# Performance work log

Measured on AMD Instinct MI355X. Metric: run time of the kernel, lower is better.

The kernel has to match this reference:

```python
import jax, jax.numpy as jnp
import numpy as np

EPS = 1e-8  # torch.nn.CosineSimilarity eps


def setup_inputs() -> dict:
    key = jax.random.key(0)
    k1, k2, k3 = jax.random.split(key, 3)
    C, S, D = 1024, 16, 512
    x = jax.random.normal(k1, (C, S, D), dtype=jnp.float32)
    w = jax.random.normal(k2, (1,), dtype=jnp.float32)
    b = jax.random.normal(k3, (1,), dtype=jnp.float32)
    return {"x": x, "w": w, "b": b}


def reference(x, w, b):
    # stable_ge2e: leave-one-out positive centroids, full negative centroids.
    C, S, D = x.shape
    wp = jax.nn.softplus(w)  # (1,)

    sum_c = x.sum(axis=1)                      # (C, D)
    mean_c = sum_c / S                         # negative centroids (C, D)
    loo = (sum_c[:, None, :] - x) / (S - 1.0)  # leave-one-out centroids (C, S, D)

    nx = jnp.linalg.norm(x, axis=-1)           # (C, S)
    nmean = jnp.linalg.norm(mean_c, axis=-1)   # (C,)
    nloo = jnp.linalg.norm(loo, axis=-1)       # (C, S)

    # cosine similarities (clamped denominator, as in torch CosineSimilarity)
    sim_neg = jnp.einsum('jid,kd->jik', x, mean_c) / jnp.maximum(
        nx[:, :, None] * nmean[None, None, :], EPS)          # (C, S, C)
    sim_pos = jnp.einsum('jid,jid->ji', x, loo) / jnp.maximum(nx * nloo, EPS)  # (C, S)

    # on the diagonal k == j use the leave-one-out positive centroid
    eye = jnp.eye(C, dtype=bool)
    sim = jnp.where(eye[:, None, :], sim_pos[:, :, None], sim_neg)  # (C, S, C)

    logits = wp * sim + b
    logS = jax.nn.log_softmax(logits, axis=-1)
    Sji_j = jnp.einsum('jij->ji', logS)                        # (C, S) diagonal
    Sji_k = jax.scipy.special.logsumexp(logS, axis=-1)         # (C, S) (== 0 post-softmax)
    loss = -(Sji_j - Sji_k).reshape(-1)
    return loss.mean()
```

## Files before the change

kernel.cpp:

```cpp
#include <hip/hip_runtime.h>
#include <math.h>

#define CC 1024
#define SS 16
#define DD 512
#define RR (CC*SS)
#define EPSV 1e-8f
#define LDB 520
#define LDX 516
#define CHUNK 32
#define NCHUNK 16

typedef __attribute__((ext_vector_type(8))) short short8;
typedef __attribute__((ext_vector_type(4))) float f32x4;
typedef unsigned short ushort_t;

__device__ __forceinline__ unsigned short f2bf(float f) {
  unsigned u = __float_as_uint(f);
  u += 0x7fffu + ((u >> 16) & 1u);
  return (unsigned short)(u >> 16);
}

__device__ __forceinline__ void async16(void* l, const void* g) {
  __builtin_amdgcn_global_load_lds(
      (const __attribute__((address_space(1))) void*)g,
      (__attribute__((address_space(3))) void*)l, 16, 0, 0);
}

__device__ __forceinline__ float softplusf(float v) {
  return (v > 20.f) ? v : log1pf(expf(v));
}

#define SBAR()   __builtin_amdgcn_s_barrier()
#define SCHED0() __builtin_amdgcn_sched_barrier(0)

__global__ __launch_bounds__(256) void k_pre(
    const float* __restrict__ x, ushort_t* __restrict__ mn,
    float* __restrict__ nx, float* __restrict__ simpos,
    ushort_t* __restrict__ xn) {
  __shared__ float xs[SS * LDX];
  __shared__ float sums[DD];
  __shared__ float red[4];
  __shared__ float snm;
  __shared__ float rinv[SS];
  const int j = blockIdx.x, tid = threadIdx.x;
  const int wid = tid >> 6, lane = tid & 63;
  const float4* xj = (const float4*)(x + (size_t)j * SS * DD);
#pragma unroll
  for (int t = 0; t < 8; ++t) {
    const int idx = tid + t * 256;
    const int row = idx >> 7, d4 = idx & 127;
    *(float4*)(xs + row * LDX + d4 * 4) = xj[idx];
  }
  __syncthreads();

  float sx = 0.f, sy = 0.f;
#pragma unroll
  for (int i = 0; i < SS; ++i) {
    float2 v = *(const float2*)(xs + i * LDX + tid * 2);
    sx += v.x; sy += v.y;
  }
  ((float2*)sums)[tid] = make_float2(sx, sy);
  const float mxs = sx * (1.0f / SS), mys = sy * (1.0f / SS);
  float m2 = mxs * mxs + mys * mys;
#pragma unroll
  for (int off = 32; off > 0; off >>= 1) m2 += __shfl_xor(m2, off, 64);
  if (lane == 0) red[wid] = m2;
  __syncthreads();
  if (tid == 0) snm = sqrtf(red[0] + red[1] + red[2] + red[3]);
  __syncthreads();
  const float inm = (1.0f / SS) / snm;
  {
    unsigned lo = f2bf(sx * inm), hi = f2bf(sy * inm);
    ((unsigned*)(mn + (size_t)j * DD))[tid] = lo | (hi << 16);
  }

  {
    const int g = tid >> 4, l16 = tid & 15;
    float nx2 = 0.f, dxs = 0.f, t2 = 0.f;
    const float2* xr2 = (const float2*)(xs + g * LDX);
    const float2* sm2 = (const float2*)sums;
#pragma unroll
    for (int t = 0; t < 16; ++t) {
      float2 xv = xr2[l16 + t * 16];
      float2 sc = sm2[l16 + t * 16];
      nx2 = fmaf(xv.x, xv.x, fmaf(xv.y, xv.y, nx2));
      dxs = fmaf(xv.x, sc.x, fmaf(xv.y, sc.y, dxs));
      float tx = sc.x - xv.x, ty = sc.y - xv.y;
      t2 = fmaf(tx, tx, fmaf(ty, ty, t2));
    }
#pragma unroll
    for (int off = 1; off < 16; off <<= 1) {
      nx2 += __shfl_xor(nx2, off, 64);
      dxs += __shfl_xor(dxs, off, 64);
      t2  += __shfl_xor(t2,  off, 64);
    }
    if (l16 == 0) {
      float nxv = sqrtf(nx2);
      float tn  = sqrtf(t2);
      float num = (dxs - nx2) * (1.0f / (SS - 1));
      float den = fmaxf(nxv * tn * (1.0f / (SS - 1)), EPSV);
      nx[j * SS + g] = nxv;
      rinv[g] = 1.0f / nxv;
      simpos[j * SS + g] = num / den;
    }
  }
  __syncthreads();
  if (xn) {
    uint4* dst = (uint4*)xn + (size_t)j * 1024;
#pragma unroll
    for (int t = 0; t < 4; ++t) {
      const int idxu = tid + t * 256;
      const int kc = idxu >> 6, quad = (idxu >> 4) & 3, cL = idxu & 15;
      const float* s = xs + cL * LDX + kc * 32 + quad * 8;
      const float4 a = *(const float4*)s;
      const float4 b2 = *(const float4*)(s + 4);
      const float ri = rinv[cL];
      uint4 o;
      o.x = (unsigned)f2bf(a.x * ri) | ((unsigned)f2bf(a.y * ri) << 16);
      o.y = (unsigned)f2bf(a.z * ri) | ((unsigned)f2bf(a.w * ri) << 16);
      o.z = (unsigned)f2bf(b2.x * ri) | ((unsigned)f2bf(b2.y * ri) << 16);
      o.w = (unsigned)f2bf(b2.z * ri) | ((unsigned)f2bf(b2.w * ri) << 16);
      dst[idxu] = o;
    }
  }
}

template <bool USE_XN>
__global__ __launch_bounds__(128, 2) void k_gemm(
    const float* __restrict__ x, const ushort_t* __restrict__ xn,
    const ushort_t* __restrict__ mn, const float* __restrict__ nx,
    const float* __restrict__ simpos, const float* __restrict__ wptr,
    const float* __restrict__ bptr, float* __restrict__ ps) {
  __shared__ ushort_t bs[2][CHUNK * LDB];
  const int tid = threadIdx.x;
  const int wid = tid >> 6, lane = tid & 63;
  const int cL = lane & 15, quad = lane >> 4;
  const int bid = (int)blockIdx.x;
  const int rb = bid & 255, cb = bid >> 8;
  const int r0 = rb * 64, cbase = cb * 512;
  const float wp = softplusf(wptr[0]), bv = bptr[0];
  const int row0w = r0 + wid * 32;

  {
    const ushort_t* gsrc = mn + (size_t)cbase * DD;
#pragma unroll
    for (int t = 0; t < 16; ++t) {
      const int rr = wid + t * 2;
      async16(&bs[0][rr * LDB + lane * 8], gsrc + (size_t)rr * DD + lane * 8);
    }
  }

  short8 af[2][16];
  int jw[2];
  float sp[2][4], sacc[2][4];
#pragma unroll
  for (int rt = 0; rt < 2; ++rt) {
    jw[rt] = (row0w + rt * 16) >> 4;
    if (USE_XN) {
      const short8* xw = (const short8*)xn + (size_t)jw[rt] * 1024;
#pragma unroll
      for (int kc = 0; kc < 16; ++kc) af[rt][kc] = xw[kc * 64 + lane];
    } else {
      const int row = row0w + rt * 16 + cL;
      const float* xr = x + (size_t)row * DD;
      const float invn = 1.0f / nx[row];
#pragma unroll
      for (int kc = 0; kc < 16; ++kc) {
        const int k0 = kc * 32 + quad * 8;
        float4 p = *(const float4*)(xr + k0);
        float4 q = *(const float4*)(xr + k0 + 4);
        short8 v;
        v[0] = f2bf(p.x * invn); v[1] = f2bf(p.y * invn);
        v[2] = f2bf(p.z * invn); v[3] = f2bf(p.w * invn);
        v[4] = f2bf(q.x * invn); v[5] = f2bf(q.y * invn);
        v[6] = f2bf(q.z * invn); v[7] = f2bf(q.w * invn);
        af[rt][kc] = v;
      }
    }
#pragma unroll
    for (int r = 0; r < 4; ++r) {
      sp[rt][r] = simpos[row0w + rt * 16 + quad * 4 + r];
      sacc[rt][r] = 0.f;
    }
  }

#pragma unroll
  for (int cc = 0; cc < NCHUNK; ++cc) {
    if (cc < NCHUNK - 1) {
      const ushort_t* gsrc = mn + (size_t)(cbase + (cc + 1) * CHUNK) * DD;
      ushort_t* dst = bs[(cc + 1) & 1];
#pragma unroll
      for (int t = 0; t < 16; ++t) {
        const int rr = wid + t * 2;
        async16(&dst[rr * LDB + lane * 8], gsrc + (size_t)rr * DD + lane * 8);
      }
      SCHED0();
      asm volatile("s_waitcnt vmcnt(16)" ::: "memory");
    } else {
      asm volatile("s_waitcnt vmcnt(0)" ::: "memory");
    }
    SCHED0();
    SBAR();
    SCHED0();

    const ushort_t* B = bs[cc & 1];
    f32x4 acc[2][2];
#pragma unroll
    for (int rt = 0; rt < 2; ++rt)
#pragma unroll
      for (int f = 0; f < 2; ++f) acc[rt][f] = (f32x4){0.f, 0.f, 0.f, 0.f};
#pragma unroll
    for (int kc = 0; kc < 16; ++kc) {
      short8 bfr[2];
#pragma unroll
      for (int f = 0; f < 2; ++f)
        bfr[f] = *(const short8*)&B[(f * 16 + cL) * LDB + kc * 32 + quad * 8];
#pragma unroll
      for (int rt = 0; rt < 2; ++rt)
#pragma unroll
        for (int f = 0; f < 2; ++f)
          acc[rt][f] = __builtin_amdgcn_mfma_f32_16x16x32_bf16(
              af[rt][kc], bfr[f], acc[rt][f], 0, 0, 0);
    }
    const int c0 = cbase + cc * CHUNK;
#pragma unroll
    for (int rt = 0; rt < 2; ++rt)
#pragma unroll
      for (int f = 0; f < 2; ++f) {
        const int cg = c0 + f * 16 + cL;
        const bool diag = (cg == jw[rt]);
#pragma unroll
        for (int r = 0; r < 4; ++r) {
          const float sim = diag ? sp[rt][r] : acc[rt][f][r];
          sacc[rt][r] += __expf(fmaf(wp, sim, bv));
        }
      }
    if (cc < NCHUNK - 1) {
      SCHED0();
      SBAR();
      SCHED0();
    }
  }

#pragma unroll
  for (int rt = 0; rt < 2; ++rt)
#pragma unroll
    for (int r = 0; r < 4; ++r) {
      float v = sacc[rt][r];
#pragma unroll
      for (int off = 1; off < 16; off <<= 1) v += __shfl_xor(v, off, 64);
      if (cL == 0)
        ps[(size_t)(row0w + rt * 16 + quad * 4 + r) * 2 + cb] = v;
    }
}

__global__ __launch_bounds__(256) void k_combine(
    const float* __restrict__ ps, const float* __restrict__ simpos,
    const float* __restrict__ wptr, const float* __restrict__ bptr,
    float* __restrict__ p2) {
  __shared__ float red[4];
  const int tid = threadIdx.x;
  const int row = blockIdx.x * 256 + tid;
  const float wp = softplusf(wptr[0]), bv = bptr[0];
  const float2 v2 = ((const float2*)ps)[row];
  float v = logf(v2.x + v2.y) - fmaf(wp, simpos[row], bv);
#pragma unroll
  for (int off = 32; off > 0; off >>= 1) v += __shfl_xor(v, off, 64);
  if ((tid & 63) == 0) red[tid >> 6] = v;
  __syncthreads();
  if (tid == 0) p2[blockIdx.x] = red[0] + red[1] + red[2] + red[3];
}

__global__ __launch_bounds__(64) void k_fin(const float* __restrict__ p2,
                                            float* __restrict__ out) {
  const int tid = threadIdx.x;
  float v = p2[tid];
#pragma unroll
  for (int off = 32; off > 0; off >>= 1) v += __shfl_xor(v, off, 64);
  if (tid == 0) out[0] = v * (1.0f / RR);
}

extern "C" void kernel_launch(void* const* d_in, const int* in_sizes, int n_in,
                              void* d_out, int out_size, void* d_ws, size_t ws_size,
                              hipStream_t stream) {
  const float* x = (const float*)d_in[0];
  const float* w = (const float*)d_in[1];
  const float* b = (const float*)d_in[2];
  float* out = (float*)d_out;

  const size_t xn_bytes = (size_t)RR * DD * 2;
  const size_t rest = (size_t)CC * DD * 2 + (size_t)RR * 4 * 2 +
                      (size_t)RR * 2 * 4 + 64 * 4;
  const bool use_xn = ws_size >= xn_bytes + rest + 256;

  char* base = (char*)d_ws;
  ushort_t* xn = use_xn ? (ushort_t*)base : nullptr;
  char* p = base + (use_xn ? xn_bytes : 0);
  ushort_t* mn = (ushort_t*)p;  p += (size_t)CC * DD * 2;
  float* nx     = (float*)p;    p += (size_t)RR * 4;
  float* simpos = (float*)p;    p += (size_t)RR * 4;
  float* ps     = (float*)p;    p += (size_t)RR * 2 * 4;
  float* p2     = (float*)p;

  k_pre<<<CC, 256, 0, stream>>>(x, mn, nx, simpos, xn);
  if (use_xn)
    k_gemm<true><<<512, 128, 0, stream>>>(x, xn, mn, nx, simpos, w, b, ps);
  else
    k_gemm<false><<<512, 128, 0, stream>>>(x, xn, mn, nx, simpos, w, b, ps);
  k_combine<<<RR / 256, 256, 0, stream>>>(ps, simpos, w, b, p2);
  k_fin<<<1, 64, 0, stream>>>(p2, out);
}
```

Before: 110.1 us.

## Fuse preprocessing and GEMM into one persistent kernel with grid barrier

Merges the per-speaker preprocessing kernel and the bf16 MFMA similarity kernel into a single 256-block kernel. Each block handles 8 speakers. It builds their normalized bf16 A-fragments directly in registers from double-buffered async LDS loads, so the xn and nx intermediates are no longer written to and read back from global memory. An atomic counter grid barrier then waits until all centroids (mn) are written before the GEMM phase starts. This removes a launch and the intermediate traffic, but doubles the preprocessing work across the two column halves, halves the grid, and relies on all 256 blocks being co-resident to avoid deadlock.

```diff
diff --git a/kernel.cpp b/kernel.cpp
--- a/kernel.cpp
+++ b/kernel.cpp
@@ -34,154 +34,156 @@
 #define SBAR()   __builtin_amdgcn_s_barrier()
 #define SCHED0() __builtin_amdgcn_sched_barrier(0)
 
-__global__ __launch_bounds__(256) void k_pre(
+__global__ __launch_bounds__(256, 1) void k_fused(
     const float* __restrict__ x, ushort_t* __restrict__ mn,
-    float* __restrict__ nx, float* __restrict__ simpos,
-    ushort_t* __restrict__ xn) {
-  __shared__ float xs[SS * LDX];
+    float* __restrict__ simpos, const float* __restrict__ wptr,
+    const float* __restrict__ bptr, float* __restrict__ ps,
+    unsigned* __restrict__ cnt) {
+  __shared__ char smem[88064];
   __shared__ float sums[DD];
   __shared__ float red[4];
   __shared__ float snm;
   __shared__ float rinv[SS];
-  const int j = blockIdx.x, tid = threadIdx.x;
-  const int wid = tid >> 6, lane = tid & 63;
-  const float4* xj = (const float4*)(x + (size_t)j * SS * DD);
-#pragma unroll
-  for (int t = 0; t < 8; ++t) {
-    const int idx = tid + t * 256;
-    const int row = idx >> 7, d4 = idx & 127;
-    *(float4*)(xs + row * LDX + d4 * 4) = xj[idx];
-  }
-  __syncthreads();
-
-  float sx = 0.f, sy = 0.f;
-#pragma unroll
-  for (int i = 0; i < SS; ++i) {
-    float2 v = *(const float2*)(xs + i * LDX + tid * 2);
-    sx += v.x; sy += v.y;
-  }
-  ((float2*)sums)[tid] = make_float2(sx, sy);
-  const float mxs = sx * (1.0f / SS), mys = sy * (1.0f / SS);
-  float m2 = mxs * mxs + mys * mys;
-#pragma unroll
-  for (int off = 32; off > 0; off >>= 1) m2 += __shfl_xor(m2, off, 64);
-  if (lane == 0) red[wid] = m2;
-  __syncthreads();
-  if (tid == 0) snm = sqrtf(red[0] + red[1] + red[2] + red[3]);
-  __syncthreads();
-  const float inm = (1.0f / SS) / snm;
-  {
-    unsigned lo = f2bf(sx * inm), hi = f2bf(sy * inm);
-    ((unsigned*)(mn + (size_t)j * DD))[tid] = lo | (hi << 16);
-  }
-
-  {
-    const int g = tid >> 4, l16 = tid & 15;
-    float nx2 = 0.f, dxs = 0.f, t2 = 0.f;
-    const float2* xr2 = (const float2*)(xs + g * LDX);
-    const float2* sm2 = (const float2*)sums;
-#pragma unroll
-    for (int t = 0; t < 16; ++t) {
-      float2 xv = xr2[l16 + t * 16];
-      float2 sc = sm2[l16 + t * 16];
-      nx2 = fmaf(xv.x, xv.x, fmaf(xv.y, xv.y, nx2));
-      dxs = fmaf(xv.x, sc.x, fmaf(xv.y, sc.y, dxs));
-      float tx = sc.x - xv.x, ty = sc.y - xv.y;
-      t2 = fmaf(tx, tx, fmaf(ty, ty, t2));
-    }
-#pragma unroll
-    for (int off = 1; off < 16; off <<= 1) {
-      nx2 += __shfl_xor(nx2, off, 64);
-      dxs += __shfl_xor(dxs, off, 64);
-      t2  += __shfl_xor(t2,  off, 64);
-    }
-    if (l16 == 0) {
-      float nxv = sqrtf(nx2);
-      float tn  = sqrtf(t2);
-      float num = (dxs - nx2) * (1.0f / (SS - 1));
-      float den = fmaxf(nxv * tn * (1.0f / (SS - 1)), EPSV);
-      nx[j * SS + g] = nxv;
-      rinv[g] = 1.0f / nxv;
-      simpos[j * SS + g] = num / den;
-    }
-  }
-  __syncthreads();
-  if (xn) {
-    uint4* dst = (uint4*)xn + (size_t)j * 1024;
-#pragma unroll
-    for (int t = 0; t < 4; ++t) {
-      const int idxu = tid + t * 256;
-      const int kc = idxu >> 6, quad = (idxu >> 4) & 3, cL = idxu & 15;
-      const float* s = xs + cL * LDX + kc * 32 + quad * 8;
-      const float4 a = *(const float4*)s;
-      const float4 b2 = *(const float4*)(s + 4);
-      const float ri = rinv[cL];
-      uint4 o;
-      o.x = (unsigned)f2bf(a.x * ri) | ((unsigned)f2bf(a.y * ri) << 16);
-      o.y = (unsigned)f2bf(a.z * ri) | ((unsigned)f2bf(a.w * ri) << 16);
-      o.z = (unsigned)f2bf(b2.x * ri) | ((unsigned)f2bf(b2.y * ri) << 16);
-      o.w = (unsigned)f2bf(b2.z * ri) | ((unsigned)f2bf(b2.w * ri) << 16);
-      dst[idxu] = o;
-    }
-  }
-}
-
-template <bool USE_XN>
-__global__ __launch_bounds__(128, 2) void k_gemm(
-    const float* __restrict__ x, const ushort_t* __restrict__ xn,
-    const ushort_t* __restrict__ mn, const float* __restrict__ nx,
-    const float* __restrict__ simpos, const float* __restrict__ wptr,
-    const float* __restrict__ bptr, float* __restrict__ ps) {
-  __shared__ ushort_t bs[2][CHUNK * LDB];
+  __shared__ float spos[SS];
+
   const int tid = threadIdx.x;
   const int wid = tid >> 6, lane = tid & 63;
   const int cL = lane & 15, quad = lane >> 4;
   const int bid = (int)blockIdx.x;
-  const int rb = bid & 255, cb = bid >> 8;
-  const int r0 = rb * 64, cbase = cb * 512;
+  const int p = bid >> 1, cb = bid & 1;
+  const int r0 = p * 128, cbase = cb * 512;
+  const int row0w = r0 + wid * 32;
   const float wp = softplusf(wptr[0]), bv = bptr[0];
-  const int row0w = r0 + wid * 32;
-
-  {
-    const ushort_t* gsrc = mn + (size_t)cbase * DD;
-#pragma unroll
-    for (int t = 0; t < 16; ++t) {
-      const int rr = wid + t * 2;
-      async16(&bs[0][rr * LDB + lane * 8], gsrc + (size_t)rr * DD + lane * 8);
-    }
-  }
+
+  float* xs0 = (float*)smem;
+  float* xs1 = (float*)smem + SS * LDX;
 
   short8 af[2][16];
   int jw[2];
   float sp[2][4], sacc[2][4];
 #pragma unroll
   for (int rt = 0; rt < 2; ++rt) {
-    jw[rt] = (row0w + rt * 16) >> 4;
-    if (USE_XN) {
-      const short8* xw = (const short8*)xn + (size_t)jw[rt] * 1024;
-#pragma unroll
-      for (int kc = 0; kc < 16; ++kc) af[rt][kc] = xw[kc * 64 + lane];
+    jw[rt] = p * 8 + 2 * wid + rt;
+#pragma unroll
+    for (int r4 = 0; r4 < 4; ++r4) sacc[rt][r4] = 0.f;
+  }
+
+  auto stage1 = [&](int r, float* dstb) {
+    const float* src = x + (size_t)(p * 8 + r) * SS * DD;
+#pragma unroll
+    for (int t = 0; t < 8; ++t) {
+      const int u0 = wid * 64 + t * 256;
+      const int row = u0 >> 7, d4 = u0 & 127;
+      async16(&dstb[row * LDX + d4 * 4 + lane * 4],
+              src + (size_t)row * DD + d4 * 4 + lane * 4);
+    }
+  };
+
+  stage1(0, xs0);
+  for (int r = 0; r < 8; ++r) {
+    float* xb = (r & 1) ? xs1 : xs0;
+    if (r < 7) {
+      stage1(r + 1, (r & 1) ? xs0 : xs1);
+      SCHED0();
+      asm volatile("s_waitcnt vmcnt(8)" ::: "memory");
     } else {
-      const int row = row0w + rt * 16 + cL;
-      const float* xr = x + (size_t)row * DD;
-      const float invn = 1.0f / nx[row];
+      asm volatile("s_waitcnt vmcnt(0)" ::: "memory");
+    }
+    SCHED0();
+    __syncthreads();
+
+    const int jc = p * 8 + r;
+    float sx = 0.f, sy = 0.f;
+#pragma unroll
+    for (int i = 0; i < SS; ++i) {
+      float2 v = *(const float2*)(xb + i * LDX + tid * 2);
+      sx += v.x; sy += v.y;
+    }
+    ((float2*)sums)[tid] = make_float2(sx, sy);
+    const float mxs = sx * (1.0f / SS), mys = sy * (1.0f / SS);
+    float m2 = mxs * mxs + mys * mys;
+#pragma unroll
+    for (int off = 32; off > 0; off >>= 1) m2 += __shfl_xor(m2, off, 64);
+    if (lane == 0) red[wid] = m2;
+    __syncthreads();
+    if (tid == 0) snm = sqrtf(red[0] + red[1] + red[2] + red[3]);
+    __syncthreads();
+    if (cb == 0) {
+      const float inm = (1.0f / SS) / snm;
+      unsigned lo = f2bf(sx * inm), hi = f2bf(sy * inm);
+      ((unsigned*)(mn + (size_t)jc * DD))[tid] = lo | (hi << 16);
+    }
+    {
+      const int g = tid >> 4, l16 = tid & 15;
+      float nx2 = 0.f, dxs = 0.f, t2 = 0.f;
+      const float2* xr2 = (const float2*)(xb + g * LDX);
+      const float2* sm2 = (const float2*)sums;
+#pragma unroll
+      for (int t = 0; t < 16; ++t) {
+        float2 xv = xr2[l16 + t * 16];
+        float2 sc = sm2[l16 + t * 16];
+        nx2 = fmaf(xv.x, xv.x, fmaf(xv.y, xv.y, nx2));
+        dxs = fmaf(xv.x, sc.x, fmaf(xv.y, sc.y, dxs));
+        float tx = sc.x - xv.x, ty = sc.y - xv.y;
+        t2 = fmaf(tx, tx, fmaf(ty, ty, t2));
+      }
+#pragma unroll
+      for (int off = 1; off < 16; off <<= 1) {
+        nx2 += __shfl_xor(nx2, off, 64);
+        dxs += __shfl_xor(dxs, off, 64);
+        t2  += __shfl_xor(t2,  off, 64);
+      }
+      if (l16 == 0) {
+        float nxv = sqrtf(nx2);
+        float tn  = sqrtf(t2);
+        float num = (dxs - nx2) * (1.0f / (SS - 1));
+        float den = fmaxf(nxv * tn * (1.0f / (SS - 1)), EPSV);
+        rinv[g] = 1.0f / nxv;
+        float spv = num / den;
+        spos[g] = spv;
+        if (cb == 0) simpos[jc * SS + g] = spv;
+      }
+    }
+    __syncthreads();
+    if (wid == (r >> 1)) {
+      const int rt = r & 1;
+      const float ri = rinv[cL];
 #pragma unroll
       for (int kc = 0; kc < 16; ++kc) {
-        const int k0 = kc * 32 + quad * 8;
-        float4 p = *(const float4*)(xr + k0);
-        float4 q = *(const float4*)(xr + k0 + 4);
+        const float* s = xb + cL * LDX + kc * 32 + quad * 8;
+        const float4 a = *(const float4*)s;
+        const float4 b2 = *(const float4*)(s + 4);
         short8 v;
-        v[0] = f2bf(p.x * invn); v[1] = f2bf(p.y * invn);
-        v[2] = f2bf(p.z * invn); v[3] = f2bf(p.w * invn);
-        v[4] = f2bf(q.x * invn); v[5] = f2bf(q.y * invn);
-        v[6] = f2bf(q.z * invn); v[7] = f2bf(q.w * invn);
+        v[0] = f2bf(a.x * ri); v[1] = f2bf(a.y * ri);
+        v[2] = f2bf(a.z * ri); v[3] = f2bf(a.w * ri);
+        v[4] = f2bf(b2.x * ri); v[5] = f2bf(b2.y * ri);
+        v[6] = f2bf(b2.z * ri); v[7] = f2bf(b2.w * ri);
         af[rt][kc] = v;
       }
-    }
-#pragma unroll
-    for (int r = 0; r < 4; ++r) {
-      sp[rt][r] = simpos[row0w + rt * 16 + quad * 4 + r];
-      sacc[rt][r] = 0.f;
+#pragma unroll
+      for (int r4 = 0; r4 < 4; ++r4) sp[rt][r4] = spos[quad * 4 + r4];
+    }
+    __syncthreads();
+  }
+
+  if (tid == 0) {
+    __builtin_amdgcn_fence(__ATOMIC_RELEASE, "agent");
+    __hip_atomic_fetch_add(cnt, 1u, __ATOMIC_RELAXED, __HIP_MEMORY_SCOPE_AGENT);
+    while (__hip_atomic_load(cnt, __ATOMIC_RELAXED, __HIP_MEMORY_SCOPE_AGENT) <
+           (unsigned)gridDim.x)
+      __builtin_amdgcn_s_sleep(8);
+    __builtin_amdgcn_fence(__ATOMIC_ACQUIRE, "agent");
+  }
+  __syncthreads();
+
+  ushort_t (*bs)[CHUNK * LDB] = (ushort_t(*)[CHUNK * LDB])smem;
+
+  {
+    const ushort_t* gsrc = mn + (size_t)cbase * DD;
+#pragma unroll
+    for (int t = 0; t < 8; ++t) {
+      const int rr = wid + t * 4;
+      async16(&bs[0][rr * LDB + lane * 8], gsrc + (size_t)rr * DD + lane * 8);
     }
   }
 
@@ -191,12 +193,12 @@
       const ushort_t* gsrc = mn + (size_t)(cbase + (cc + 1) * CHUNK) * DD;
       ushort_t* dst = bs[(cc + 1) & 1];
 #pragma unroll
-      for (int t = 0; t < 16; ++t) {
-        const int rr = wid + t * 2;
+      for (int t = 0; t < 8; ++t) {
+        const int rr = wid + t * 4;
         async16(&dst[rr * LDB + lane * 8], gsrc + (size_t)rr * DD + lane * 8);
       }
       SCHED0();
-      asm volatile("s_waitcnt vmcnt(16)" ::: "memory");
+      asm volatile("s_waitcnt vmcnt(8)" ::: "memory");
     } else {
       asm volatile("s_waitcnt vmcnt(0)" ::: "memory");
     }
@@ -231,9 +233,9 @@
         const int cg = c0 + f * 16 + cL;
         const bool diag = (cg == jw[rt]);
 #pragma unroll
-        for (int r = 0; r < 4; ++r) {
-          const float sim = diag ? sp[rt][r] : acc[rt][f][r];
-          sacc[rt][r] += __expf(fmaf(wp, sim, bv));
+        for (int r4 = 0; r4 < 4; ++r4) {
+          const float sim = diag ? sp[rt][r4] : acc[rt][f][r4];
+          sacc[rt][r4] += __expf(fmaf(wp, sim, bv));
         }
       }
     if (cc < NCHUNK - 1) {
@@ -246,12 +248,12 @@
 #pragma unroll
   for (int rt = 0; rt < 2; ++rt)
 #pragma unroll
-    for (int r = 0; r < 4; ++r) {
-      float v = sacc[rt][r];
+    for (int r4 = 0; r4 < 4; ++r4) {
+      float v = sacc[rt][r4];
 #pragma unroll
       for (int off = 1; off < 16; off <<= 1) v += __shfl_xor(v, off, 64);
       if (cL == 0)
-        ps[(size_t)(row0w + rt * 16 + quad * 4 + r) * 2 + cb] = v;
+        ps[(size_t)(row0w + rt * 16 + quad * 4 + r4) * 2 + cb] = v;
     }
 }
 
@@ -289,25 +291,16 @@
   const float* b = (const float*)d_in[2];
   float* out = (float*)d_out;
 
-  const size_t xn_bytes = (size_t)RR * DD * 2;
-  const size_t rest = (size_t)CC * DD * 2 + (size_t)RR * 4 * 2 +
-                      (size_t)RR * 2 * 4 + 64 * 4;
-  const bool use_xn = ws_size >= xn_bytes + rest + 256;
-
   char* base = (char*)d_ws;
-  ushort_t* xn = use_xn ? (ushort_t*)base : nullptr;
-  char* p = base + (use_xn ? xn_bytes : 0);
-  ushort_t* mn = (ushort_t*)p;  p += (size_t)CC * DD * 2;
-  float* nx     = (float*)p;    p += (size_t)RR * 4;
-  float* simpos = (float*)p;    p += (size_t)RR * 4;
-  float* ps     = (float*)p;    p += (size_t)RR * 2 * 4;
-  float* p2     = (float*)p;
-
-  k_pre<<<CC, 256, 0, stream>>>(x, mn, nx, simpos, xn);
-  if (use_xn)
-    k_gemm<true><<<512, 128, 0, stream>>>(x, xn, mn, nx, simpos, w, b, ps);
-  else
-    k_gemm<false><<<512, 128, 0, stream>>>(x, xn, mn, nx, simpos, w, b, ps);
+  unsigned* cnt = (unsigned*)base;
+  char* pp = base + 256;
+  ushort_t* mn = (ushort_t*)pp;  pp += (size_t)CC * DD * 2;
+  float* simpos = (float*)pp;    pp += (size_t)RR * 4;
+  float* ps     = (float*)pp;    pp += (size_t)RR * 2 * 4;
+  float* p2     = (float*)pp;
+
+  hipMemsetAsync(cnt, 0, 4, stream);
+  k_fused<<<256, 256, 0, stream>>>(x, mn, simpos, w, b, ps, cnt);
   k_combine<<<RR / 256, 256, 0, stream>>>(ps, simpos, w, b, p2);
   k_fin<<<1, 64, 0, stream>>>(p2, out);
 }
```

New measurement: 159.0 us. +44.4%, slower.

## Store mean centroids pre-swizzled in MFMA fragment layout and load B directly from global

Applied to the files above, without the earlier changes.

The preprocessing kernel now writes the normalized bf16 centroids in MFMA B-fragment order, so each lane's short8 for a 16-column tile is contiguous. The GEMM kernel drops the LDS double-buffered async staging and its barriers, and instead loads each tile's 16 fragments straight from global memory (L2-resident) into registers before issuing the MFMAs. This removes LDS traffic and synchronisation, but gives up cross-wave sharing of B through LDS, adds register pressure, and exposes global-load latency with no explicit prefetch.

```diff
diff --git a/kernel.cpp b/kernel.cpp
--- a/kernel.cpp
+++ b/kernel.cpp
@@ -6,10 +6,7 @@
 #define DD 512
 #define RR (CC*SS)
 #define EPSV 1e-8f
-#define LDB 520
 #define LDX 516
-#define CHUNK 32
-#define NCHUNK 16
 
 typedef __attribute__((ext_vector_type(8))) short short8;
 typedef __attribute__((ext_vector_type(4))) float f32x4;
@@ -21,21 +18,12 @@
   return (unsigned short)(u >> 16);
 }
 
-__device__ __forceinline__ void async16(void* l, const void* g) {
-  __builtin_amdgcn_global_load_lds(
-      (const __attribute__((address_space(1))) void*)g,
-      (__attribute__((address_space(3))) void*)l, 16, 0, 0);
-}
-
 __device__ __forceinline__ float softplusf(float v) {
   return (v > 20.f) ? v : log1pf(expf(v));
 }
 
-#define SBAR()   __builtin_amdgcn_s_barrier()
-#define SCHED0() __builtin_amdgcn_sched_barrier(0)
-
 __global__ __launch_bounds__(256) void k_pre(
-    const float* __restrict__ x, ushort_t* __restrict__ mn,
+    const float* __restrict__ x, ushort_t* __restrict__ mnf,
     float* __restrict__ nx, float* __restrict__ simpos,
     ushort_t* __restrict__ xn) {
   __shared__ float xs[SS * LDX];
@@ -43,6 +31,7 @@
   __shared__ float red[4];
   __shared__ float snm;
   __shared__ float rinv[SS];
+  __shared__ ushort_t mrow[DD];
   const int j = blockIdx.x, tid = threadIdx.x;
   const int wid = tid >> 6, lane = tid & 63;
   const float4* xj = (const float4*)(x + (size_t)j * SS * DD);
@@ -72,7 +61,7 @@
   const float inm = (1.0f / SS) / snm;
   {
     unsigned lo = f2bf(sx * inm), hi = f2bf(sy * inm);
-    ((unsigned*)(mn + (size_t)j * DD))[tid] = lo | (hi << 16);
+    ((unsigned*)mrow)[tid] = lo | (hi << 16);
   }
 
   {
@@ -106,6 +95,13 @@
     }
   }
   __syncthreads();
+
+  if (tid < 64) {
+    const int kc = tid >> 2, quad = tid & 3;
+    const uint4 u = *(const uint4*)&mrow[kc * 32 + quad * 8];
+    ((uint4*)mnf)[(size_t)((j >> 4) * 16 + kc) * 64 + quad * 16 + (j & 15)] = u;
+  }
+
   if (xn) {
     uint4* dst = (uint4*)xn + (size_t)j * 1024;
 #pragma unroll
@@ -129,27 +125,17 @@
 template <bool USE_XN>
 __global__ __launch_bounds__(128, 2) void k_gemm(
     const float* __restrict__ x, const ushort_t* __restrict__ xn,
-    const ushort_t* __restrict__ mn, const float* __restrict__ nx,
+    const ushort_t* __restrict__ mnf, const float* __restrict__ nx,
     const float* __restrict__ simpos, const float* __restrict__ wptr,
     const float* __restrict__ bptr, float* __restrict__ ps) {
-  __shared__ ushort_t bs[2][CHUNK * LDB];
   const int tid = threadIdx.x;
   const int wid = tid >> 6, lane = tid & 63;
   const int cL = lane & 15, quad = lane >> 4;
   const int bid = (int)blockIdx.x;
   const int rb = bid & 255, cb = bid >> 8;
-  const int r0 = rb * 64, cbase = cb * 512;
+  const int r0 = rb * 64, ft0 = cb * 32;
   const float wp = softplusf(wptr[0]), bv = bptr[0];
   const int row0w = r0 + wid * 32;
-
-  {
-    const ushort_t* gsrc = mn + (size_t)cbase * DD;
-#pragma unroll
-    for (int t = 0; t < 16; ++t) {
-      const int rr = wid + t * 2;
-      async16(&bs[0][rr * LDB + lane * 8], gsrc + (size_t)rr * DD + lane * 8);
-    }
-  }
 
   short8 af[2][16];
   int jw[2];
@@ -185,61 +171,31 @@
     }
   }
 
-#pragma unroll
-  for (int cc = 0; cc < NCHUNK; ++cc) {
-    if (cc < NCHUNK - 1) {
-      const ushort_t* gsrc = mn + (size_t)(cbase + (cc + 1) * CHUNK) * DD;
-      ushort_t* dst = bs[(cc + 1) & 1];
-#pragma unroll
-      for (int t = 0; t < 16; ++t) {
-        const int rr = wid + t * 2;
-        async16(&dst[rr * LDB + lane * 8], gsrc + (size_t)rr * DD + lane * 8);
+  const short8* bbase = (const short8*)mnf + (size_t)ft0 * 1024 + lane;
+  for (int f = 0; f < 32; ++f) {
+    const short8* bp = bbase + (size_t)f * 1024;
+    short8 bf[16];
+#pragma unroll
+    for (int kc = 0; kc < 16; ++kc) bf[kc] = bp[kc * 64];
+    f32x4 acc[2];
+#pragma unroll
+    for (int rt = 0; rt < 2; ++rt) acc[rt] = (f32x4){0.f, 0.f, 0.f, 0.f};
+#pragma unroll
+    for (int kc = 0; kc < 16; ++kc) {
+      acc[0] = __builtin_amdgcn_mfma_f32_16x16x32_bf16(af[0][kc], bf[kc],
+                                                       acc[0], 0, 0, 0);
+      acc[1] = __builtin_amdgcn_mfma_f32_16x16x32_bf16(af[1][kc], bf[kc],
+                                                       acc[1], 0, 0, 0);
+    }
+    const int cg = (ft0 + f) * 16 + cL;
+#pragma unroll
+    for (int rt = 0; rt < 2; ++rt) {
+      const bool diag = (cg == jw[rt]);
+#pragma unroll
+      for (int r = 0; r < 4; ++r) {
+        const float sim = diag ? sp[rt][r] : acc[rt][r];
+        sacc[rt][r] += __expf(fmaf(wp, sim, bv));
       }
-      SCHED0();
-      asm volatile("s_waitcnt vmcnt(16)" ::: "memory");
-    } else {
-      asm volatile("s_waitcnt vmcnt(0)" ::: "memory");
-    }
-    SCHED0();
-    SBAR();
-    SCHED0();
-
-    const ushort_t* B = bs[cc & 1];
-    f32x4 acc[2][2];
-#pragma unroll
-    for (int rt = 0; rt < 2; ++rt)
-#pragma unroll
-      for (int f = 0; f < 2; ++f) acc[rt][f] = (f32x4){0.f, 0.f, 0.f, 0.f};
-#pragma unroll
-    for (int kc = 0; kc < 16; ++kc) {
-      short8 bfr[2];
-#pragma unroll
-      for (int f = 0; f < 2; ++f)
-        bfr[f] = *(const short8*)&B[(f * 16 + cL) * LDB + kc * 32 + quad * 8];
-#pragma unroll
-      for (int rt = 0; rt < 2; ++rt)
-#pragma unroll
-        for (int f = 0; f < 2; ++f)
-          acc[rt][f] = __builtin_amdgcn_mfma_f32_16x16x32_bf16(
-              af[rt][kc], bfr[f], acc[rt][f], 0, 0, 0);
-    }
-    const int c0 = cbase + cc * CHUNK;
-#pragma unroll
-    for (int rt = 0; rt < 2; ++rt)
-#pragma unroll
-      for (int f = 0; f < 2; ++f) {
-        const int cg = c0 + f * 16 + cL;
-        const bool diag = (cg == jw[rt]);
-#pragma unroll
-        for (int r = 0; r < 4; ++r) {
-          const float sim = diag ? sp[rt][r] : acc[rt][f][r];
-          sacc[rt][r] += __expf(fmaf(wp, sim, bv));
-        }
-      }
-    if (cc < NCHUNK - 1) {
-      SCHED0();
-      SBAR();
-      SCHED0();
     }
   }
 
@@ -297,17 +253,17 @@
   char* base = (char*)d_ws;
   ushort_t* xn = use_xn ? (ushort_t*)base : nullptr;
   char* p = base + (use_xn ? xn_bytes : 0);
-  ushort_t* mn = (ushort_t*)p;  p += (size_t)CC * DD * 2;
+  ushort_t* mnf = (ushort_t*)p; p += (size_t)CC * DD * 2;
   float* nx     = (float*)p;    p += (size_t)RR * 4;
   float* simpos = (float*)p;    p += (size_t)RR * 4;
   float* ps     = (float*)p;    p += (size_t)RR * 2 * 4;
   float* p2     = (float*)p;
 
-  k_pre<<<CC, 256, 0, stream>>>(x, mn, nx, simpos, xn);
+  k_pre<<<CC, 256, 0, stream>>>(x, mnf, nx, simpos, xn);
   if (use_xn)
-    k_gemm<true><<<512, 128, 0, stream>>>(x, xn, mn, nx, simpos, w, b, ps);
+    k_gemm<true><<<512, 128, 0, stream>>>(x, xn, mnf, nx, simpos, w, b, ps);
   else
-    k_gemm<false><<<512, 128, 0, stream>>>(x, xn, mn, nx, simpos, w, b, ps);
+    k_gemm<false><<<512, 128, 0, stream>>>(x, xn, mnf, nx, simpos, w, b, ps);
   k_combine<<<RR / 256, 256, 0, stream>>>(ps, simpos, w, b, p2);
   k_fin<<<1, 64, 0, stream>>>(p2, out);
 }
```

After: 160.6 us. 45.9% more time.
